# Performance work log

Measured on AMD Instinct MI355X. Metric: run time of the kernel, lower is better.

## Reference

```python
import jax, jax.numpy as jnp
import numpy as np

B, T, H = 8, 512, 1024
DC = 8            # concept_dim_total = 6 + 2
DIN = H + DC      # 1032
V, L = 8, 4       # op_vocab_size, prog_len


def setup_inputs() -> dict:
    key = jax.random.key(0)
    ks = jax.random.split(key, 20)
    s = 0.02
    inp = {
        "x": jax.random.normal(ks[0], (B, T, H), dtype=jnp.float32),
        # concept classifier heads
        "W_tt": jax.random.normal(ks[1], (6, H), dtype=jnp.float32) * s,
        "b_tt": jnp.zeros((6,), jnp.float32),
        "W_pol": jax.random.normal(ks[2], (2, H), dtype=jnp.float32) * s,
        "b_pol": jnp.zeros((2,), jnp.float32),
        # program generator
        "W_c2h": jax.random.normal(ks[3], (H, DIN), dtype=jnp.float32) * s,
        "b_c2h": jnp.zeros((H,), jnp.float32),
        "W_ih": jax.random.normal(ks[4], (3 * H, DIN), dtype=jnp.float32) * s,
        "W_hh": jax.random.normal(ks[5], (3 * H, H), dtype=jnp.float32) * s,
        "b_ih": jnp.zeros((3 * H,), jnp.float32),
        "b_hh": jnp.zeros((3 * H,), jnp.float32),
        "W_proj": jax.random.normal(ks[6], (V, H), dtype=jnp.float32) * s,
        "b_proj": jnp.zeros((V,), jnp.float32),
        # op library: num_ops stacked Linear(DIN->H)-GELU-Linear(H->H)
        "W1": jax.random.normal(ks[7], (V, H, DIN), dtype=jnp.float32) * s,
        "b1": jnp.zeros((V, H), jnp.float32),
        "W2": jax.random.normal(ks[8], (V, H, H), dtype=jnp.float32) * s,
        "b2": jnp.zeros((V, H), jnp.float32),
    }
    return inp


def _forward(x, W_tt, b_tt, W_pol, b_pol, W_c2h, b_c2h, W_ih, W_hh, b_ih, b_hh,
             W_proj, b_proj, W1, b1, W2, b2):
    # concept classifier
    tt = x @ W_tt.T + b_tt              # (B,T,6)
    pol = x @ W_pol.T + b_pol           # (B,T,2)
    concept_feats = jnp.concatenate([tt, pol], axis=-1)  # (B,T,8)
    concept_summary = jnp.concatenate([tt.mean(axis=1), pol.mean(axis=1)], axis=-1)  # (B,8)
    pooled = x.mean(axis=1)             # (B,H)
    context = jnp.concatenate([pooled, concept_summary], axis=-1)  # (B,DIN)

    # program generator: GRU with zero inputs, h0 from context (PyTorch gate eqs)
    h0 = context @ W_c2h.T + b_c2h      # (B,H)
    zero_in = jnp.zeros((context.shape[0], DIN), x.dtype)
    gi = zero_in @ W_ih.T + b_ih        # (B,3H); zero-input contribution = bias
    gi_r, gi_z, gi_n = jnp.split(gi, 3, axis=-1)

    def gru_step(h, _):
        gh = h @ W_hh.T + b_hh
        gh_r, gh_z, gh_n = jnp.split(gh, 3, axis=-1)
        r = jax.nn.sigmoid(gi_r + gh_r)
        z = jax.nn.sigmoid(gi_z + gh_z)
        n = jnp.tanh(gi_n + r * gh_n)
        h_new = (1.0 - z) * n + z * h
        return h_new, h_new

    _, hs = jax.lax.scan(gru_step, h0, None, length=L)   # (L,B,H)
    rnn_out = jnp.transpose(hs, (1, 0, 2))               # (B,L,H)
    program_logits = rnn_out @ W_proj.T + b_proj         # (B,L,V)

    # op library: outputs are identical across L, so compute each op once and
    # average the softmax weights over L (exact same math as expand+mean).
    x_aug = jnp.concatenate([x, concept_feats], axis=-1)           # (B,T,DIN)
    hmid = jax.nn.gelu(jnp.einsum('btd,vhd->btvh', x_aug, W1) + b1, approximate=False)
    op_out = jnp.einsum('btvh,voh->btvo', hmid, W2) + b2           # (B,T,V,H)
    w = jax.nn.softmax(program_logits, axis=-1).mean(axis=1)       # (B,V)
    out = jnp.einsum('btvd,bv->btd', op_out, w)                    # (B,T,H)
    return out, program_logits, tt, pol, pooled


def reference(x, W_tt, b_tt, W_pol, b_pol, W_c2h, b_c2h, W_ih, W_hh, b_ih, b_hh,
              W_proj, b_proj, W1, b1, W2, b2):
    return _forward(x, W_tt, b_tt, W_pol, b_pol, W_c2h, b_c2h, W_ih, W_hh,
                    b_ih, b_hh, W_proj, b_proj, W1, b1, W2, b2)
```

## Files before the change

### kernel.cpp

```cpp
#include <hip/hip_runtime.h>
#include <hip/hip_bf16.h>
#include <math.h>

typedef __bf16 bf16;
typedef __bf16 bf16x8 __attribute__((ext_vector_type(8)));
typedef float f32x4 __attribute__((ext_vector_type(4)));


__device__ __forceinline__ float wsum(float v) {
#pragma unroll
  for (int off = 32; off; off >>= 1) v += __shfl_xor(v, off, 64);
  return v;
}

__device__ __forceinline__ void g2l16(const bf16* g, bf16* l) {
  __builtin_amdgcn_global_load_lds(
      (__attribute__((address_space(1))) void*)g,
      (__attribute__((address_space(3))) void*)l, 16, 0, 0);
}

__device__ __forceinline__ bf16x8 pack8(float4 a, float4 b) {
  bf16x8 r;
  r[0] = (bf16)a.x; r[1] = (bf16)a.y; r[2] = (bf16)a.z; r[3] = (bf16)a.w;
  r[4] = (bf16)b.x; r[5] = (bf16)b.y; r[6] = (bf16)b.z; r[7] = (bf16)b.w;
  return r;
}

__device__ __forceinline__ float gelu_fast(float x) {
  float s = __builtin_fabsf(x) * 0.70710678118654752f;
  float t = __builtin_amdgcn_rcpf(__builtin_fmaf(0.3275911f, s, 1.0f));
  float p = __builtin_fmaf(t, 1.061405429f, -1.453152027f);
  p = __builtin_fmaf(t, p, 1.421413741f);
  p = __builtin_fmaf(t, p, -0.284496736f);
  p = __builtin_fmaf(t, p, 0.254829592f);
  float e = exp2f(s * s * -1.4426950408889634f);
  float erf_abs = __builtin_fmaf(-p * t, e, 1.0f);
  return __builtin_fmaf(0.5f * __builtin_fabsf(x), erf_abs, 0.5f * x);
}

template <int DCT>
__global__ void k_front_t(const float* __restrict__ x,
                          const float* __restrict__ Wtt, const float* __restrict__ btt,
                          const float* __restrict__ Wpol, const float* __restrict__ bpol,
                          float* __restrict__ out_tt, float* __restrict__ out_pol,
                          float* __restrict__ feats, bf16* __restrict__ xbE,
                          int H, int KE, long BT, int C1, int C2) {
  int wave = threadIdx.x >> 6, lane = threadIdx.x & 63;
  long m = (long)blockIdx.x * 4 + wave;
  if (m >= BT) return;
  const float* xp = x + m * H;
  bf16* dp = xbE + m * KE;
  const float* wp[DCT];
#pragma unroll
  for (int c = 0; c < DCT; c++)
    wp[c] = (c < C1) ? (Wtt + (size_t)c * H) : (Wpol + (size_t)(c - C1) * H);
  float acc[DCT];
#pragma unroll
  for (int c = 0; c < DCT; c++) acc[c] = 0.f;
  for (int e = lane * 8; e + 8 <= H; e += 512) {
    float4 a = *(const float4*)(xp + e);
    float4 b = *(const float4*)(xp + e + 4);
    *(bf16x8*)(dp + e) = pack8(a, b);
#pragma unroll
    for (int c = 0; c < DCT; c++) {
      float4 wa = *(const float4*)(wp[c] + e);
      float4 wb = *(const float4*)(wp[c] + e + 4);
      acc[c] += a.x * wa.x + a.y * wa.y + a.z * wa.z + a.w * wa.w +
                b.x * wb.x + b.y * wb.y + b.z * wb.z + b.w * wb.w;
    }
  }
#pragma unroll
  for (int c = 0; c < DCT; c++) acc[c] = wsum(acc[c]);
  float fv = 0.f;
#pragma unroll
  for (int c = 0; c < DCT; c++) fv = (lane == c) ? acc[c] : fv;
  if (lane < DCT) {
    fv += (lane < C1) ? btt[lane] : bpol[lane - C1];
    if (lane < C1) out_tt[m * C1 + lane] = fv;
    else           out_pol[m * C2 + (lane - C1)] = fv;
    feats[m * DCT + lane] = fv;
  }
  int pad = KE - H;
  if (lane < pad) dp[H + lane] = (lane < DCT) ? (bf16)fv : (bf16)0.f;
}

__global__ void k_feats_g(const float* __restrict__ x,
                          const float* __restrict__ Wtt, const float* __restrict__ btt,
                          const float* __restrict__ Wpol, const float* __restrict__ bpol,
                          float* __restrict__ out_tt, float* __restrict__ out_pol,
                          float* __restrict__ feats,
                          int H, int T, int BT, int C1, int C2) {
  int wave = threadIdx.x >> 6, lane = threadIdx.x & 63;
  int site = blockIdx.x * 4 + wave;
  if (site >= BT) return;
  int DC = C1 + C2;
  const float* xp = x + (size_t)site * H;
  for (int c = 0; c < DC; c++) {
    const float* wr = (c < C1) ? (Wtt + (size_t)c * H) : (Wpol + (size_t)(c - C1) * H);
    float a = 0.f;
    for (int k = lane; k < H; k += 64) a += xp[k] * wr[k];
    a = wsum(a);
    if (lane == 0) {
      float val = a + (c < C1 ? btt[c] : bpol[c - C1]);
      if (c < C1) out_tt[(size_t)site * C1 + c] = val;
      else        out_pol[(size_t)site * C2 + (c - C1)] = val;
      feats[(size_t)site * DC + c] = val;
    }
  }
}

__global__ void k_xext(const float* __restrict__ x, const float* __restrict__ feats,
                       bf16* __restrict__ xbE, int H, int KE, int DC, long BT) {
  int wave = threadIdx.x >> 6, lane = threadIdx.x & 63;
  long m = (long)blockIdx.x * 4 + wave;
  if (m >= BT) return;
  const float* xp = x + m * H;
  bf16* dp = xbE + m * KE;
  for (int e = lane * 8; e + 8 <= H; e += 512) {
    float4 a = *(const float4*)(xp + e);
    float4 b = *(const float4*)(xp + e + 4);
    *(bf16x8*)(dp + e) = pack8(a, b);
  }
  int pad = KE - H;
  if (lane < pad)
    dp[H + lane] = (lane < DC) ? (bf16)feats[m * DC + lane] : (bf16)0.f;
}

__global__ void k_prep(const float* __restrict__ W1, bf16* __restrict__ W1bE,
                       const float* __restrict__ W2, bf16* __restrict__ W2b,
                       int H, int DIN, int KE, int DC, long N2, int nW1, long nCvtThreads) {
  int wave = threadIdx.x >> 6, lane = threadIdx.x & 63;
  if (blockIdx.x < (unsigned)nW1) {
    long n = (long)blockIdx.x * 4 + wave;
    if (n >= N2) return;
    const float* sp = W1 + n * DIN;
    bf16* dp = W1bE + n * KE;
    for (int e = lane * 8; e + 8 <= H; e += 512) {
      float4 a = *(const float4*)(sp + e);
      float4 b = *(const float4*)(sp + e + 4);
      *(bf16x8*)(dp + e) = pack8(a, b);
    }
    int pad = KE - H;
    if (lane < pad)
      dp[H + lane] = (lane < DC) ? (bf16)sp[H + lane] : (bf16)0.f;
  } else {
    long n = N2 * (long)H;
    for (long i = (long)(blockIdx.x - nW1) * 256 + threadIdx.x; i * 8 < n;
         i += nCvtThreads) {
      long e = i * 8;
      if (e + 8 <= n) {
        float4 a = *(const float4*)(W2 + e);
        float4 b = *(const float4*)(W2 + e + 4);
        *(bf16x8*)(W2b + e) = pack8(a, b);
      } else {
        for (long j = e; j < n; j++) W2b[j] = (bf16)W2[j];
      }
    }
  }
}

__global__ void k_stats(const float* __restrict__ x, float* __restrict__ pooled,
                        const float* __restrict__ feats, float* __restrict__ fsum,
                        int H, int T, int tsplit, int DC, int BDC, int poolBlocks) {
  int wave = threadIdx.x >> 6, lane = threadIdx.x & 63;
  if (blockIdx.x < (unsigned)poolBlocks) {
    int hBlocks = (H + 255) / 256;
    int bs = blockIdx.x / tsplit, ts = blockIdx.x % tsplit;
    int b = bs / hBlocks;
    int h = (bs % hBlocks) * 256 + threadIdx.x;
    if (h >= H) return;
    int tlo = (int)(((long)T * ts) / tsplit), thi = (int)(((long)T * (ts + 1)) / tsplit);
    const float* p = x + (size_t)b * T * H + h;
    float s = 0.f;
    for (int t = tlo; t < thi; t++) s += p[(size_t)t * H];
    atomicAdd(&pooled[(size_t)b * H + h], s / (float)T);
  } else {
    int r = (blockIdx.x - poolBlocks) * 4 + wave;
    if (r >= BDC) return;
    int b = r / DC, c = r % DC;
    const float* p = feats + ((size_t)b * T) * DC + c;
    float a = 0.f;
    for (int t = lane; t < T; t += 64) a += p[(size_t)t * DC];
    a = wsum(a);
    if (lane == 0) fsum[r] = a / (float)T;
  }
}

__global__ void k_ctx_h0(const float* __restrict__ Wc2h, const float* __restrict__ bc2h,
                         const float* __restrict__ pooled, const float* __restrict__ fmean,
                         float* __restrict__ h0, float* __restrict__ out_pool,
                         int H, int DIN, int B, int DC) {
  int wave = threadIdx.x >> 6, lane = threadIdx.x & 63;
  int r = blockIdx.x * 4 + wave;
  if (r >= B * H) return;
  int b = r / H, j = r % H;
  const float* wrow = Wc2h + (size_t)j * DIN;
  float a = 0.f;
  for (int k = lane; k < DIN; k += 64) {
    float cv = (k < H) ? pooled[(size_t)b * H + k] : fmean[b * DC + (k - H)];
    a += cv * wrow[k];
  }
  a = wsum(a);
  if (lane == 0) {
    h0[r] = a + bc2h[j];
    out_pool[r] = pooled[r];
  }
}

__global__ void k_gru(const float* __restrict__ hin, const float* __restrict__ Whh,
                      const float* __restrict__ bih, const float* __restrict__ bhh,
                      float* __restrict__ hout, float* __restrict__ hsl,
                      int H, int B) {
  int wave = threadIdx.x >> 6, lane = threadIdx.x & 63;
  int r = blockIdx.x * 4 + wave;
  if (r >= B * H) return;
  int b = r / H, j = r % H;
  const float* h = hin + (size_t)b * H;
  const float* w0 = Whh + (size_t)j * H;
  const float* w1 = Whh + (size_t)(H + j) * H;
  const float* w2 = Whh + (size_t)(2 * H + j) * H;
  float ar = 0, az = 0, an = 0;
  for (int k = lane; k < H; k += 64) {
    float hv = h[k];
    ar += hv * w0[k];
    az += hv * w1[k];
    an += hv * w2[k];
  }
  ar = wsum(ar); az = wsum(az); an = wsum(an);
  if (lane == 0) {
    float ghr = ar + bhh[j];
    float ghz = az + bhh[H + j];
    float ghn = an + bhh[2 * H + j];
    float rg = 1.f / (1.f + expf(-(bih[j] + ghr)));
    float zg = 1.f / (1.f + expf(-(bih[H + j] + ghz)));
    float ng = tanhf(bih[2 * H + j] + rg * ghn);
    float hn = (1.f - zg) * ng + zg * h[j];
    hout[r] = hn;
    hsl[r] = hn;
  }
}

__global__ void k_logits(const float* __restrict__ hs, const float* __restrict__ Wproj,
                         const float* __restrict__ bproj, float* __restrict__ logits,
                         float* __restrict__ out_log, int H, int B, int L, int V) {
  int wave = threadIdx.x >> 6, lane = threadIdx.x & 63;
  int r = blockIdx.x * 4 + wave;
  if (r >= B * L * V) return;
  int b = r / (L * V), rem = r % (L * V), l = rem / V, u = rem % V;
  const float* h = hs + ((size_t)l * B + b) * H;
  const float* w = Wproj + (size_t)u * H;
  float a = 0.f;
  for (int k = lane; k < H; k += 64) a += h[k] * w[k];
  a = wsum(a);
  if (lane == 0) {
    a += bproj[u];
    int idx = (b * L + l) * V + u;
    logits[idx] = a;
    out_log[idx] = a;
  }
}

__global__ void k_wmix(const float* __restrict__ logits, const float* __restrict__ b2,
                       float* __restrict__ wv, float* __restrict__ wb2,
                       int B, int L, int V, int H) {
  __shared__ float sm[2048];
  __shared__ float wsh[512];
  int t = threadIdx.x;
  if (t < B * L) {
    const float* lg = logits + t * V;
    float mx = lg[0];
    for (int u = 1; u < V; u++) mx = fmaxf(mx, lg[u]);
    float s = 0.f;
    for (int u = 0; u < V; u++) s += expf(lg[u] - mx);
    for (int u = 0; u < V; u++) sm[t * V + u] = expf(lg[u] - mx) / s;
  }
  __syncthreads();
  if (t < B * V) {
    int b = t / V, u = t % V;
    float a = 0.f;
    for (int l = 0; l < L; l++) a += sm[(b * L + l) * V + u];
    a /= (float)L;
    wsh[t] = a;
    wv[t] = a;
  }
  __syncthreads();
  for (int idx = t; idx < B * H; idx += 256) {
    int b = idx / H, o = idx % H;
    float a = 0.f;
    for (int u = 0; u < V; u++) a += wsh[b * V + u] * b2[(size_t)u * H + o];
    wb2[idx] = a;
  }
}

__global__ __launch_bounds__(256, 2) void gemm1_mfma(
    const bf16* __restrict__ A, const bf16* __restrict__ Bb, bf16* __restrict__ hmid,
    const float* __restrict__ b1, const float* __restrict__ wv,
    int rows, long moff, int KE, int H, int N, int T, int V) {
  __shared__ __align__(16) bf16 As[128 * 64];
  __shared__ __align__(16) bf16 Bs[128 * 64];
  const int wave = threadIdx.x >> 6, lane = threadIdx.x & 63;
  int bx = blockIdx.x, by = blockIdx.y;
  if (gridDim.x == 64 && (gridDim.y & 3) == 0) {
    int f = by * 64 + bx;
    int xcd = f & 7, q = f >> 3;
    int cs = q >> 5, t = q & 31;
    bx = xcd * 8 + (t & 7);
    by = cs * 4 + (t >> 3);
  }
  const int m0 = by * 128, n0 = bx * 128;
  const int mw = (wave >> 1) * 64, nw = (wave & 1) * 64;
  const int rr = lane >> 3;
  const int srcOff = ((lane & 7) ^ rr) << 3;
  const int rA = lane & 15, q4 = lane >> 4;
  f32x4 acc[4][4];
#pragma unroll
  for (int i = 0; i < 4; i++)
#pragma unroll
    for (int j = 0; j < 4; j++) acc[i][j] = (f32x4){0.f, 0.f, 0.f, 0.f};

  int arow[4], brow[4];
#pragma unroll
  for (int t = 0; t < 4; ++t) {
    int r = wave * 32 + t * 8 + rr;
    arow[t] = (m0 + r < rows) ? (m0 + r) : (rows - 1);
    brow[t] = (n0 + r < N) ? (n0 + r) : (N - 1);
  }

  for (int k0 = 0; k0 < KE; k0 += 64) {
    __syncthreads();
#pragma unroll
    for (int t = 0; t < 4; ++t) {
      int c = wave * 4 + t;
      g2l16(A + (size_t)arow[t] * KE + k0 + srcOff, &As[c * 512]);
      g2l16(Bb + (size_t)brow[t] * KE + k0 + srcOff, &Bs[c * 512]);
    }
    __syncthreads();
#pragma unroll
    for (int kk = 0; kk < 2; ++kk) {
      bf16x8 af[4], bfr[4];
#pragma unroll
      for (int i = 0; i < 4; i++) {
        int row = mw + i * 16 + rA;
        af[i] = *(const bf16x8*)&As[row * 64 + ((((kk << 2) + q4) ^ (row & 7)) << 3)];
      }
#pragma unroll
      for (int j = 0; j < 4; j++) {
        int row = nw + j * 16 + rA;
        bfr[j] = *(const bf16x8*)&Bs[row * 64 + ((((kk << 2) + q4) ^ (row & 7)) << 3)];
      }
#pragma unroll
      for (int i = 0; i < 4; i++)
#pragma unroll
        for (int j = 0; j < 4; j++)
          acc[i][j] = __builtin_amdgcn_mfma_f32_16x16x32_bf16(af[i], bfr[j], acc[i][j], 0, 0, 0);
    }
  }

  int vj[4];
  float b1j[4];
#pragma unroll
  for (int j = 0; j < 4; j++) {
    int n = n0 + nw + j * 16 + rA;
    if (n >= N) n = N - 1;
    vj[j] = n / H;
    b1j[j] = b1[n];
  }
  int bBase = ((T & 127) == 0) ? (int)((moff + m0) / T) : -1;
  float wfac[4];
#pragma unroll
  for (int j = 0; j < 4; j++)
    wfac[j] = (bBase >= 0) ? wv[bBase * V + vj[j]] : 0.f;
#pragma unroll
  for (int i = 0; i < 4; i++) {
#pragma unroll
    for (int r = 0; r < 4; r++) {
      int m = m0 + mw + i * 16 + q4 * 4 + r;
      if (m >= rows) continue;
      long gm = moff + m;
      int bb = (bBase >= 0) ? bBase : (int)(gm / T);
#pragma unroll
      for (int j = 0; j < 4; j++) {
        int n = n0 + nw + j * 16 + rA;
        if (n >= N) continue;
        float val = gelu_fast(acc[i][j][r] + b1j[j]);
        float wf = (bBase >= 0) ? wfac[j] : wv[bb * V + vj[j]];
        hmid[(size_t)m * N + n] = (bf16)(val * wf);
      }
    }
  }
}

__global__ __launch_bounds__(256, 2) void gemm2_mfma(
    const bf16* __restrict__ A, const bf16* __restrict__ W2b, float* __restrict__ part,
    long partStride, int rows, int H, int K, int kchunk) {
  __shared__ __align__(16) bf16 As[128 * 64];
  __shared__ __align__(16) bf16 Bs[128 * 64];
  const int wave = threadIdx.x >> 6, lane = threadIdx.x & 63;
  int bx = blockIdx.x, by = blockIdx.y;
  if (gridDim.x == 8 && (gridDim.y & 31) == 0) {
    int f = by * 8 + bx;
    int xcd = f & 7, q = f >> 3;
    int cs = q >> 5, t = q & 31;
    bx = t & 7;
    by = (xcd + (cs << 3)) * 4 + (t >> 3);
  }
  const int m0 = by * 128, n0 = bx * 128;
  const int mw = (wave >> 1) * 64, nw = (wave & 1) * 64;
  const int rr = lane >> 3;
  const int srcOff = ((lane & 7) ^ rr) << 3;
  const int rA = lane & 15, q4 = lane >> 4;
  int kz0 = blockIdx.z * kchunk;
  int kz1 = kz0 + kchunk; if (kz1 > K) kz1 = K;
  if (kz0 >= K) return;
  f32x4 acc[4][4];
#pragma unroll
  for (int i = 0; i < 4; i++)
#pragma unroll
    for (int j = 0; j < 4; j++) acc[i][j] = (f32x4){0.f, 0.f, 0.f, 0.f};

  int arow[4], brow[4];
#pragma unroll
  for (int t = 0; t < 4; ++t) {
    int r = wave * 32 + t * 8 + rr;
    arow[t] = (m0 + r < rows) ? (m0 + r) : (rows - 1);
    brow[t] = (n0 + r < H) ? (n0 + r) : (H - 1);
  }

  int kv = kz0 / H, kh = kz0 % H;
  for (int k0 = kz0; k0 < kz1; k0 += 64) {
    const bf16* Bk = W2b + (size_t)kv * H * H + kh;
    __syncthreads();
#pragma unroll
    for (int t = 0; t < 4; ++t) {
      int c = wave * 4 + t;
      g2l16(A + (size_t)arow[t] * K + k0 + srcOff, &As[c * 512]);
      g2l16(Bk + (size_t)brow[t] * H + srcOff, &Bs[c * 512]);
    }
    __syncthreads();
#pragma unroll
    for (int kk = 0; kk < 2; ++kk) {
      bf16x8 af[4], bfr[4];
#pragma unroll
      for (int i = 0; i < 4; i++) {
        int row = mw + i * 16 + rA;
        af[i] = *(const bf16x8*)&As[row * 64 + ((((kk << 2) + q4) ^ (row & 7)) << 3)];
      }
#pragma unroll
      for (int j = 0; j < 4; j++) {
        int row = nw + j * 16 + rA;
        bfr[j] = *(const bf16x8*)&Bs[row * 64 + ((((kk << 2) + q4) ^ (row & 7)) << 3)];
      }
#pragma unroll
      for (int i = 0; i < 4; i++)
#pragma unroll
        for (int j = 0; j < 4; j++)
          acc[i][j] = __builtin_amdgcn_mfma_f32_16x16x32_bf16(af[i], bfr[j], acc[i][j], 0, 0, 0);
    }
    kh += 64;
    if (kh >= H) { kh = 0; kv++; }
  }

  float* pz = part + (size_t)blockIdx.z * partStride;
#pragma unroll
  for (int i = 0; i < 4; i++) {
#pragma unroll
    for (int r = 0; r < 4; r++) {
      int m = m0 + mw + i * 16 + q4 * 4 + r;
      if (m >= rows) continue;
#pragma unroll
      for (int j = 0; j < 4; j++) {
        int n = n0 + nw + j * 16 + rA;
        if (n >= H) continue;
        pz[(size_t)m * H + n] = acc[i][j][r];
      }
    }
  }
}

__global__ void k_red(const float* __restrict__ part, const float* __restrict__ wb2,
                      float* __restrict__ outY, long moff, int rows, long partStride,
                      int H, int T, int ZS) {
  int wave = threadIdx.x >> 6, lane = threadIdx.x & 63;
  long m = (long)blockIdx.x * 4 + wave;
  if (m >= rows) return;
  long gm = moff + m;
  int b = (int)(gm / T);
  const float* w = wb2 + (size_t)b * H;
  float* d = outY + (size_t)gm * H;
  for (int e = lane * 4; e + 4 <= H; e += 256) {
    float4 s = *(const float4*)(w + e);
    for (int z = 0; z < ZS; z++) {
      float4 p = *(const float4*)(part + (size_t)z * partStride + (size_t)m * H + e);
      s.x += p.x; s.y += p.y; s.z += p.z; s.w += p.w;
    }
    *(float4*)(d + e) = s;
  }
}

extern "C" void kernel_launch(void* const* d_in, const int* in_sizes, int n_in,
                              void* d_out, int out_size, void* d_ws, size_t ws_size,
                              hipStream_t stream) {
  const float* x      = (const float*)d_in[0];
  const float* W_tt   = (const float*)d_in[1];
  const float* b_tt   = (const float*)d_in[2];
  const float* W_pol  = (const float*)d_in[3];
  const float* b_pol  = (const float*)d_in[4];
  const float* W_c2h  = (const float*)d_in[5];
  const float* b_c2h  = (const float*)d_in[6];
  const float* W_hh   = (const float*)d_in[8];
  const float* b_ih   = (const float*)d_in[9];
  const float* b_hh   = (const float*)d_in[10];
  const float* W_proj = (const float*)d_in[11];
  const float* b_proj = (const float*)d_in[12];
  const float* W1     = (const float*)d_in[13];
  const float* b1     = (const float*)d_in[14];
  const float* W2     = (const float*)d_in[15];
  const float* b2     = (const float*)d_in[16];
  float* out = (float*)d_out;
  char* ws = (char*)d_ws;

  const int C1 = in_sizes[2];
  const int C2 = in_sizes[4];
  const int H  = in_sizes[1] / C1;
  const int DC = C1 + C2;
  const int DIN = H + DC;
  const int V  = in_sizes[12];
  const long BT = (long)in_sizes[0] / H;
  long R = (long)out_size - BT * (long)(H + DC);
  int B = 0, L = 0;
  for (int Lc = 1; Lc <= 32; ++Lc) {
    long den = (long)Lc * V + H;
    if (R % den == 0) {
      long Bc = R / den;
      if (Bc >= 1 && BT % Bc == 0) {
        if (B == 0 || Lc == 4) { B = (int)Bc; L = Lc; }
        if (Lc == 4) break;
      }
    }
  }
  if (B == 0) { B = 8; L = 4; }
  const int T = (int)(BT / B);
  const long N2 = (long)V * H;
  const int KE = H + 64;
  const int ZS = 4;

  size_t o = 0;
  auto alloc = [&](size_t bytes) { size_t r = o; o = (o + bytes + 255) & ~(size_t)255; return r; };
  float* feats  = (float*)(ws + alloc((size_t)BT * DC * 4));
  size_t off_pooled = alloc((size_t)B * H * 4);
  float* pooled = (float*)(ws + off_pooled);
  float* fsum   = (float*)(ws + alloc((size_t)B * DC * 4));
  float* hbuf   = (float*)(ws + alloc((size_t)2 * B * H * 4));
  float* hs     = (float*)(ws + alloc((size_t)L * B * H * 4));
  float* logits = (float*)(ws + alloc((size_t)B * L * V * 4));
  float* wv     = (float*)(ws + alloc((size_t)B * V * 4));
  float* wb2    = (float*)(ws + alloc((size_t)B * H * 4));
  bf16* xbE  = (bf16*)(ws + alloc((size_t)BT * KE * 2));
  bf16* W1bE = (bf16*)(ws + alloc((size_t)N2 * KE * 2));
  bf16* W2b  = (bf16*)(ws + alloc((size_t)N2 * H * 2));
  size_t off_hmid = alloc(0);
  long rowBytes = N2 * 2 + (long)ZS * H * 4;
  long avail = (long)ws_size - (long)off_hmid;
  long Mc = ((avail / rowBytes) / 128) * 128;
  long bt128 = ((BT + 127) / 128) * 128;
  if (Mc > bt128) Mc = bt128;
  if (Mc < 128) Mc = 128;
  bf16* hmid = (bf16*)(ws + off_hmid);
  float* part = (float*)(ws + off_hmid + (size_t)Mc * N2 * 2);
  long partStride = Mc * (long)H;

  float* out_y    = out;
  float* out_log  = out_y + (size_t)BT * H;
  float* out_tt   = out_log + (size_t)B * L * V;
  float* out_pol  = out_tt + (size_t)BT * C1;
  float* out_pool = out_pol + (size_t)BT * C2;

  hipMemsetAsync(ws + off_pooled, 0, (size_t)B * H * 4, stream);

  int nW1 = (int)((N2 + 3) / 4);
  int nCvt = 1024;
  k_prep<<<nW1 + nCvt, 256, 0, stream>>>(W1, W1bE, W2, W2b, H, DIN, KE, DC, N2,
                                         nW1, (long)nCvt * 256);
  if (DC == 8 && (H & 1023) == 0) {
    k_front_t<8><<<(int)((BT + 3) / 4), 256, 0, stream>>>(x, W_tt, b_tt, W_pol, b_pol,
                                                          out_tt, out_pol, feats, xbE,
                                                          H, KE, BT, C1, C2);
  } else {
    k_feats_g<<<(int)((BT + 3) / 4), 256, 0, stream>>>(x, W_tt, b_tt, W_pol, b_pol,
                                                       out_tt, out_pol, feats,
                                                       H, T, (int)BT, C1, C2);
    k_xext<<<(int)((BT + 3) / 4), 256, 0, stream>>>(x, feats, xbE, H, KE, DC, BT);
  }
  int hBlocks = (H + 255) / 256;
  int poolBlocks = B * hBlocks * 8;
  int fsumBlocks = (B * DC + 3) / 4;
  k_stats<<<poolBlocks + fsumBlocks, 256, 0, stream>>>(x, pooled, feats, fsum,
                                                       H, T, 8, DC, B * DC, poolBlocks);
  k_ctx_h0<<<(B * H + 3) / 4, 256, 0, stream>>>(W_c2h, b_c2h, pooled, fsum,
                                                hbuf, out_pool, H, DIN, B, DC);
  float* hA = hbuf;
  float* hB = hbuf + (size_t)B * H;
  for (int l = 0; l < L; ++l) {
    k_gru<<<(B * H + 3) / 4, 256, 0, stream>>>((l & 1) ? hB : hA, W_hh, b_ih, b_hh,
                                               (l & 1) ? hA : hB, hs + (size_t)l * B * H,
                                               H, B);
  }
  k_logits<<<(B * L * V + 3) / 4, 256, 0, stream>>>(hs, W_proj, b_proj, logits,
                                                    out_log, H, B, L, V);
  k_wmix<<<1, 256, 0, stream>>>(logits, b2, wv, wb2, B, L, V, H);

  int kchunk = (int)((((N2 / ZS) + 63) / 64) * 64);
  for (long moff = 0; moff < BT; moff += Mc) {
    int rows = (int)(((BT - moff) < Mc) ? (BT - moff) : Mc);
    dim3 g1((unsigned)((N2 + 127) / 128), (unsigned)((rows + 127) / 128));
    dim3 g2((unsigned)((H + 127) / 128), (unsigned)((rows + 127) / 128), ZS);
    gemm1_mfma<<<g1, 256, 0, stream>>>(xbE + (size_t)moff * KE, W1bE, hmid, b1, wv,
                                       rows, moff, KE, H, (int)N2, T, V);
    gemm2_mfma<<<g2, 256, 0, stream>>>(hmid, W2b, part, partStride,
                                       rows, H, (int)N2, kchunk);
    k_red<<<(int)((rows + 3) / 4), 256, 0, stream>>>(part, wb2, out_y, moff, rows,
                                                     partStride, H, T, ZS);
  }
}
```

Baseline: 454.9 us.

## Double-buffer LDS tiles in both MFMA GEMMs with async prefetch pipeline

Both GEMM kernels now keep two LDS buffers for A and B. The next K tile is fetched with global_load_lds while the current tile is computed, and explicit vmcnt waits plus raw barriers replace the two __syncthreads per iteration, so global-load latency can overlap MFMA work. LDS use doubles to 64KB per block, which may limit the two-blocks-per-CU occupancy target. The front kernel is also reworked: the bf16 conversion loop is split from the concept dot products, which now run over float4 chunks with a stride of 256.

```diff
diff --git a/kernel.cpp b/kernel.cpp
--- a/kernel.cpp
+++ b/kernel.cpp
@@ -50,23 +50,24 @@
   if (m >= BT) return;
   const float* xp = x + m * H;
   bf16* dp = xbE + m * KE;
-  const float* wp[DCT];
-#pragma unroll
-  for (int c = 0; c < DCT; c++)
-    wp[c] = (c < C1) ? (Wtt + (size_t)c * H) : (Wpol + (size_t)(c - C1) * H);
-  float acc[DCT];
-#pragma unroll
-  for (int c = 0; c < DCT; c++) acc[c] = 0.f;
   for (int e = lane * 8; e + 8 <= H; e += 512) {
     float4 a = *(const float4*)(xp + e);
     float4 b = *(const float4*)(xp + e + 4);
     *(bf16x8*)(dp + e) = pack8(a, b);
+  }
+  const float* wp[DCT];
+#pragma unroll
+  for (int c = 0; c < DCT; c++)
+    wp[c] = (c < C1) ? (Wtt + (size_t)c * H) : (Wpol + (size_t)(c - C1) * H);
+  float acc[DCT];
+#pragma unroll
+  for (int c = 0; c < DCT; c++) acc[c] = 0.f;
+  for (int k = lane * 4; k < H; k += 256) {
+    float4 xv = *(const float4*)(xp + k);
 #pragma unroll
     for (int c = 0; c < DCT; c++) {
-      float4 wa = *(const float4*)(wp[c] + e);
-      float4 wb = *(const float4*)(wp[c] + e + 4);
-      acc[c] += a.x * wa.x + a.y * wa.y + a.z * wa.z + a.w * wa.w +
-                b.x * wb.x + b.y * wb.y + b.z * wb.z + b.w * wb.w;
+      float4 wv4 = *(const float4*)(wp[c] + k);
+      acc[c] += xv.x * wv4.x + xv.y * wv4.y + xv.z * wv4.z + xv.w * wv4.w;
     }
   }
 #pragma unroll
@@ -296,8 +297,8 @@
     const bf16* __restrict__ A, const bf16* __restrict__ Bb, bf16* __restrict__ hmid,
     const float* __restrict__ b1, const float* __restrict__ wv,
     int rows, long moff, int KE, int H, int N, int T, int V) {
-  __shared__ __align__(16) bf16 As[128 * 64];
-  __shared__ __align__(16) bf16 Bs[128 * 64];
+  __shared__ __align__(16) bf16 As[2][128 * 64];
+  __shared__ __align__(16) bf16 Bs[2][128 * 64];
   const int wave = threadIdx.x >> 6, lane = threadIdx.x & 63;
   int bx = blockIdx.x, by = blockIdx.y;
   if (gridDim.x == 64 && (gridDim.y & 3) == 0) {
@@ -326,27 +327,30 @@
     brow[t] = (n0 + r < N) ? (n0 + r) : (N - 1);
   }
 
-  for (int k0 = 0; k0 < KE; k0 += 64) {
-    __syncthreads();
+  const int NT = KE >> 6;
+  int k0s = 0;
+  auto STAGE = [&](int bsel) {
 #pragma unroll
     for (int t = 0; t < 4; ++t) {
       int c = wave * 4 + t;
-      g2l16(A + (size_t)arow[t] * KE + k0 + srcOff, &As[c * 512]);
-      g2l16(Bb + (size_t)brow[t] * KE + k0 + srcOff, &Bs[c * 512]);
-    }
-    __syncthreads();
+      g2l16(A + (size_t)arow[t] * KE + k0s + srcOff, &As[bsel][c * 512]);
+      g2l16(Bb + (size_t)brow[t] * KE + k0s + srcOff, &Bs[bsel][c * 512]);
+    }
+    k0s += 64;
+  };
+  auto COMPUTE = [&](int bsel) {
 #pragma unroll
     for (int kk = 0; kk < 2; ++kk) {
       bf16x8 af[4], bfr[4];
 #pragma unroll
       for (int i = 0; i < 4; i++) {
         int row = mw + i * 16 + rA;
-        af[i] = *(const bf16x8*)&As[row * 64 + ((((kk << 2) + q4) ^ (row & 7)) << 3)];
+        af[i] = *(const bf16x8*)&As[bsel][row * 64 + ((((kk << 2) + q4) ^ (row & 7)) << 3)];
       }
 #pragma unroll
       for (int j = 0; j < 4; j++) {
         int row = nw + j * 16 + rA;
-        bfr[j] = *(const bf16x8*)&Bs[row * 64 + ((((kk << 2) + q4) ^ (row & 7)) << 3)];
+        bfr[j] = *(const bf16x8*)&Bs[bsel][row * 64 + ((((kk << 2) + q4) ^ (row & 7)) << 3)];
       }
 #pragma unroll
       for (int i = 0; i < 4; i++)
@@ -354,7 +358,35 @@
         for (int j = 0; j < 4; j++)
           acc[i][j] = __builtin_amdgcn_mfma_f32_16x16x32_bf16(af[i], bfr[j], acc[i][j], 0, 0, 0);
     }
-  }
+  };
+
+  STAGE(0);
+  if (NT > 1) {
+    STAGE(1);
+    asm volatile("s_waitcnt vmcnt(8)" ::: "memory");
+  } else {
+    asm volatile("s_waitcnt vmcnt(0)" ::: "memory");
+  }
+  __builtin_amdgcn_s_barrier();
+  int cur = 0, t = 0;
+  for (; t + 2 < NT; ++t) {
+    COMPUTE(cur);
+    asm volatile("" ::: "memory");
+    __builtin_amdgcn_s_barrier();
+    STAGE(cur);
+    asm volatile("s_waitcnt vmcnt(8)" ::: "memory");
+    __builtin_amdgcn_s_barrier();
+    cur ^= 1;
+  }
+  if (t + 1 < NT) {
+    COMPUTE(cur);
+    asm volatile("" ::: "memory");
+    __builtin_amdgcn_s_barrier();
+    asm volatile("s_waitcnt vmcnt(0)" ::: "memory");
+    __builtin_amdgcn_s_barrier();
+    cur ^= 1;
+  }
+  COMPUTE(cur);
 
   int vj[4];
   float b1j[4];
@@ -393,8 +425,8 @@
 __global__ __launch_bounds__(256, 2) void gemm2_mfma(
     const bf16* __restrict__ A, const bf16* __restrict__ W2b, float* __restrict__ part,
     long partStride, int rows, int H, int K, int kchunk) {
-  __shared__ __align__(16) bf16 As[128 * 64];
-  __shared__ __align__(16) bf16 Bs[128 * 64];
+  __shared__ __align__(16) bf16 As[2][128 * 64];
+  __shared__ __align__(16) bf16 Bs[2][128 * 64];
   const int wave = threadIdx.x >> 6, lane = threadIdx.x & 63;
   int bx = blockIdx.x, by = blockIdx.y;
   if (gridDim.x == 8 && (gridDim.y & 31) == 0) {
@@ -426,29 +458,31 @@
     brow[t] = (n0 + r < H) ? (n0 + r) : (H - 1);
   }
 
-  int kv = kz0 / H, kh = kz0 % H;
-  for (int k0 = kz0; k0 < kz1; k0 += 64) {
-    const bf16* Bk = W2b + (size_t)kv * H * H + kh;
-    __syncthreads();
+  const int NT = (kz1 - kz0) >> 6;
+  int k0s = kz0, kvs = kz0 / H, khs = kz0 % H;
+  auto STAGE = [&](int bsel) {
+    const bf16* Bk = W2b + (size_t)kvs * H * H + khs;
 #pragma unroll
     for (int t = 0; t < 4; ++t) {
       int c = wave * 4 + t;
-      g2l16(A + (size_t)arow[t] * K + k0 + srcOff, &As[c * 512]);
-      g2l16(Bk + (size_t)brow[t] * H + srcOff, &Bs[c * 512]);
-    }
-    __syncthreads();
+      g2l16(A + (size_t)arow[t] * K + k0s + srcOff, &As[bsel][c * 512]);
+      g2l16(Bk + (size_t)brow[t] * H + srcOff, &Bs[bsel][c * 512]);
+    }
+    k0s += 64; khs += 64; if (khs >= H) { khs = 0; kvs++; }
+  };
+  auto COMPUTE = [&](int bsel) {
 #pragma unroll
     for (int kk = 0; kk < 2; ++kk) {
       bf16x8 af[4], bfr[4];
 #pragma unroll
       for (int i = 0; i < 4; i++) {
         int row = mw + i * 16 + rA;
-        af[i] = *(const bf16x8*)&As[row * 64 + ((((kk << 2) + q4) ^ (row & 7)) << 3)];
+        af[i] = *(const bf16x8*)&As[bsel][row * 64 + ((((kk << 2) + q4) ^ (row & 7)) << 3)];
       }
 #pragma unroll
       for (int j = 0; j < 4; j++) {
         int row = nw + j * 16 + rA;
-        bfr[j] = *(const bf16x8*)&Bs[row * 64 + ((((kk << 2) + q4) ^ (row & 7)) << 3)];
+        bfr[j] = *(const bf16x8*)&Bs[bsel][row * 64 + ((((kk << 2) + q4) ^ (row & 7)) << 3)];
       }
 #pragma unroll
       for (int i = 0; i < 4; i++)
@@ -456,9 +490,35 @@
         for (int j = 0; j < 4; j++)
           acc[i][j] = __builtin_amdgcn_mfma_f32_16x16x32_bf16(af[i], bfr[j], acc[i][j], 0, 0, 0);
     }
-    kh += 64;
-    if (kh >= H) { kh = 0; kv++; }
-  }
+  };
+
+  STAGE(0);
+  if (NT > 1) {
+    STAGE(1);
+    asm volatile("s_waitcnt vmcnt(8)" ::: "memory");
+  } else {
+    asm volatile("s_waitcnt vmcnt(0)" ::: "memory");
+  }
+  __builtin_amdgcn_s_barrier();
+  int cur = 0, t = 0;
+  for (; t + 2 < NT; ++t) {
+    COMPUTE(cur);
+    asm volatile("" ::: "memory");
+    __builtin_amdgcn_s_barrier();
+    STAGE(cur);
+    asm volatile("s_waitcnt vmcnt(8)" ::: "memory");
+    __builtin_amdgcn_s_barrier();
+    cur ^= 1;
+  }
+  if (t + 1 < NT) {
+    COMPUTE(cur);
+    asm volatile("" ::: "memory");
+    __builtin_amdgcn_s_barrier();
+    asm volatile("s_waitcnt vmcnt(0)" ::: "memory");
+    __builtin_amdgcn_s_barrier();
+    cur ^= 1;
+  }
+  COMPUTE(cur);
 
   float* pz = part + (size_t)blockIdx.z * partStride;
 #pragma unroll
```

Result: slower. 475.3 us (+4.5%).

## Fuse stats, h0, GRU steps, logits and softmax mix into one cooperative kernel

Applied to the files above, without the earlier changes.

Replaces the chain of small launches (pooling stats, context-to-h0, four GRU step kernels, logits, weight mix) with a single cooperative kernel of 256 blocks that uses grid-wide syncs between phases. The goal is to remove per-launch overhead and the memset on the latency-bound RNN path. In exchange each GRU row is computed by fewer waves, and grid.sync adds its own cost. The front kernel is also reordered so the bf16 copy pass and the concept dot-product pass run as separate loops with float4 strides.

```diff
diff --git a/kernel.cpp b/kernel.cpp
--- a/kernel.cpp
+++ b/kernel.cpp
@@ -1,6 +1,9 @@
 #include <hip/hip_runtime.h>
+#include <hip/hip_cooperative_groups.h>
 #include <hip/hip_bf16.h>
 #include <math.h>
+
+namespace cg = cooperative_groups;
 
 typedef __bf16 bf16;
 typedef __bf16 bf16x8 __attribute__((ext_vector_type(8)));
@@ -50,23 +53,24 @@
   if (m >= BT) return;
   const float* xp = x + m * H;
   bf16* dp = xbE + m * KE;
-  const float* wp[DCT];
-#pragma unroll
-  for (int c = 0; c < DCT; c++)
-    wp[c] = (c < C1) ? (Wtt + (size_t)c * H) : (Wpol + (size_t)(c - C1) * H);
-  float acc[DCT];
-#pragma unroll
-  for (int c = 0; c < DCT; c++) acc[c] = 0.f;
   for (int e = lane * 8; e + 8 <= H; e += 512) {
     float4 a = *(const float4*)(xp + e);
     float4 b = *(const float4*)(xp + e + 4);
     *(bf16x8*)(dp + e) = pack8(a, b);
+  }
+  const float* wp[DCT];
+#pragma unroll
+  for (int c = 0; c < DCT; c++)
+    wp[c] = (c < C1) ? (Wtt + (size_t)c * H) : (Wpol + (size_t)(c - C1) * H);
+  float acc[DCT];
+#pragma unroll
+  for (int c = 0; c < DCT; c++) acc[c] = 0.f;
+  for (int k = lane * 4; k < H; k += 256) {
+    float4 xv = *(const float4*)(xp + k);
 #pragma unroll
     for (int c = 0; c < DCT; c++) {
-      float4 wa = *(const float4*)(wp[c] + e);
-      float4 wb = *(const float4*)(wp[c] + e + 4);
-      acc[c] += a.x * wa.x + a.y * wa.y + a.z * wa.z + a.w * wa.w +
-                b.x * wb.x + b.y * wb.y + b.z * wb.z + b.w * wb.w;
+      float4 wv4 = *(const float4*)(wp[c] + k);
+      acc[c] += xv.x * wv4.x + xv.y * wv4.y + xv.z * wv4.z + xv.w * wv4.w;
     }
   }
 #pragma unroll
@@ -155,6 +159,141 @@
       } else {
         for (long j = e; j < n; j++) W2b[j] = (bf16)W2[j];
       }
+    }
+  }
+}
+
+__global__ void k_rnn(const float* __restrict__ x, const float* __restrict__ feats,
+                      float* __restrict__ pooledPart, float* __restrict__ pooled,
+                      float* __restrict__ fsum,
+                      const float* __restrict__ Wc2h, const float* __restrict__ bc2h,
+                      const float* __restrict__ Whh, const float* __restrict__ bih,
+                      const float* __restrict__ bhh,
+                      const float* __restrict__ Wproj, const float* __restrict__ bproj,
+                      const float* __restrict__ b2,
+                      float* __restrict__ hbuf, float* __restrict__ hs,
+                      float* __restrict__ out_log, float* __restrict__ wv,
+                      float* __restrict__ wb2, float* __restrict__ out_pool,
+                      int H, int DIN, int T, int B, int DC, int L, int V) {
+  cg::grid_group grid = cg::this_grid();
+  __shared__ float sm[256];
+  __shared__ float wsh[64];
+  const int bl = blockIdx.x, tid = threadIdx.x;
+  const int wave = tid >> 6, lane = tid & 63;
+  const int gw = bl * 4 + wave;
+
+  {
+    int b = bl >> 5, ts = (bl >> 2) & 7, hc = bl & 3;
+    int h = hc * 256 + tid;
+    int tlo = (int)(((long)T * ts) / 8), thi = (int)(((long)T * (ts + 1)) / 8);
+    const float* p = x + ((size_t)b * T + tlo) * H + h;
+    float s = 0.f;
+    for (int t = tlo; t < thi; t++, p += H) s += *p;
+    pooledPart[((size_t)ts * B + b) * H + h] = s;
+  }
+  grid.sync();
+  {
+    int idx = bl * 256 + tid;
+    if (idx < B * H) {
+      float s = 0.f;
+      for (int ts = 0; ts < 8; ts++) s += pooledPart[(size_t)ts * B * H + idx];
+      s /= (float)T;
+      pooled[idx] = s;
+      out_pool[idx] = s;
+    }
+    int r = (bl - 32) * 4 + wave;
+    if (bl >= 32 && r < B * DC) {
+      int b = r / DC, c = r % DC;
+      const float* p = feats + ((size_t)b * T) * DC + c;
+      float a = 0.f;
+      for (int t = lane; t < T; t += 64) a += p[(size_t)t * DC];
+      a = wsum(a);
+      if (lane == 0) fsum[r] = a / (float)T;
+    }
+  }
+  grid.sync();
+  float* hA = hbuf;
+  float* hB = hbuf + (size_t)B * H;
+  for (int w = 0; w < 8; w++) {
+    int r = gw * 8 + w;
+    if (r >= B * H) break;
+    int b = r / H, j = r % H;
+    const float* wrow = Wc2h + (size_t)j * DIN;
+    float a = 0.f;
+    for (int k = lane; k < DIN; k += 64) {
+      float cv = (k < H) ? pooled[(size_t)b * H + k] : fsum[b * DC + (k - H)];
+      a += cv * wrow[k];
+    }
+    a = wsum(a);
+    if (lane == 0) hA[r] = a + bc2h[j];
+  }
+  grid.sync();
+  for (int l = 0; l < L; l++) {
+    const float* hin = (l & 1) ? hB : hA;
+    float* hout = (l & 1) ? hA : hB;
+    for (int w = 0; w < 8; w++) {
+      int r = gw * 8 + w;
+      if (r >= B * H) break;
+      int b = r / H, j = r % H;
+      const float* h = hin + (size_t)b * H;
+      const float* w0 = Whh + (size_t)j * H;
+      const float* w1 = Whh + (size_t)(H + j) * H;
+      const float* w2 = Whh + (size_t)(2 * H + j) * H;
+      float ar = 0, az = 0, an = 0;
+      for (int k = lane; k < H; k += 64) {
+        float hv = h[k];
+        ar += hv * w0[k];
+        az += hv * w1[k];
+        an += hv * w2[k];
+      }
+      ar = wsum(ar); az = wsum(az); an = wsum(an);
+      if (lane == 0) {
+        float ghr = ar + bhh[j];
+        float ghz = az + bhh[H + j];
+        float ghn = an + bhh[2 * H + j];
+        float rg = 1.f / (1.f + expf(-(bih[j] + ghr)));
+        float zg = 1.f / (1.f + expf(-(bih[H + j] + ghz)));
+        float ng = tanhf(bih[2 * H + j] + rg * ghn);
+        float hn = (1.f - zg) * ng + zg * h[j];
+        hout[r] = hn;
+        hs[(size_t)l * B * H + r] = hn;
+      }
+    }
+    grid.sync();
+  }
+  if (gw < B * L * V) {
+    int b = gw / (L * V), rem = gw % (L * V), l = rem / V, u = rem % V;
+    const float* h = hs + ((size_t)l * B + b) * H;
+    const float* wp = Wproj + (size_t)u * H;
+    float a = 0.f;
+    for (int k = lane; k < H; k += 64) a += h[k] * wp[k];
+    a = wsum(a);
+    if (lane == 0) out_log[(b * L + l) * V + u] = a + bproj[u];
+  }
+  grid.sync();
+  if (bl < B) {
+    int b = bl;
+    if (tid < L) {
+      const float* lg = out_log + (b * L + tid) * V;
+      float mx = lg[0];
+      for (int u = 1; u < V; u++) mx = fmaxf(mx, lg[u]);
+      float s = 0.f;
+      for (int u = 0; u < V; u++) s += expf(lg[u] - mx);
+      for (int u = 0; u < V; u++) sm[tid * V + u] = expf(lg[u] - mx) / s;
+    }
+    __syncthreads();
+    if (tid < V) {
+      float a = 0.f;
+      for (int l = 0; l < L; l++) a += sm[l * V + tid];
+      a /= (float)L;
+      wsh[tid] = a;
+      wv[b * V + tid] = a;
+    }
+    __syncthreads();
+    for (int o = tid; o < H; o += 256) {
+      float a = 0.f;
+      for (int u = 0; u < V; u++) a += wsh[u] * b2[(size_t)u * H + o];
+      wb2[(size_t)b * H + o] = a;
     }
   }
 }
@@ -550,6 +689,7 @@
   size_t off_pooled = alloc((size_t)B * H * 4);
   float* pooled = (float*)(ws + off_pooled);
   float* fsum   = (float*)(ws + alloc((size_t)B * DC * 4));
+  float* pooledPart = (float*)(ws + alloc((size_t)8 * B * H * 4));
   float* hbuf   = (float*)(ws + alloc((size_t)2 * B * H * 4));
   float* hs     = (float*)(ws + alloc((size_t)L * B * H * 4));
   float* logits = (float*)(ws + alloc((size_t)B * L * V * 4));
@@ -575,13 +715,12 @@
   float* out_pol  = out_tt + (size_t)BT * C1;
   float* out_pool = out_pol + (size_t)BT * C2;
 
-  hipMemsetAsync(ws + off_pooled, 0, (size_t)B * H * 4, stream);
-
   int nW1 = (int)((N2 + 3) / 4);
   int nCvt = 1024;
   k_prep<<<nW1 + nCvt, 256, 0, stream>>>(W1, W1bE, W2, W2b, H, DIN, KE, DC, N2,
                                          nW1, (long)nCvt * 256);
-  if (DC == 8 && (H & 1023) == 0) {
+  bool frontFused = (DC == 8 && (H & 1023) == 0);
+  if (frontFused) {
     k_front_t<8><<<(int)((BT + 3) / 4), 256, 0, stream>>>(x, W_tt, b_tt, W_pol, b_pol,
                                                           out_tt, out_pol, feats, xbE,
                                                           H, KE, BT, C1, C2);
@@ -591,23 +730,37 @@
                                                        H, T, (int)BT, C1, C2);
     k_xext<<<(int)((BT + 3) / 4), 256, 0, stream>>>(x, feats, xbE, H, KE, DC, BT);
   }
-  int hBlocks = (H + 255) / 256;
-  int poolBlocks = B * hBlocks * 8;
-  int fsumBlocks = (B * DC + 3) / 4;
-  k_stats<<<poolBlocks + fsumBlocks, 256, 0, stream>>>(x, pooled, feats, fsum,
-                                                       H, T, 8, DC, B * DC, poolBlocks);
-  k_ctx_h0<<<(B * H + 3) / 4, 256, 0, stream>>>(W_c2h, b_c2h, pooled, fsum,
-                                                hbuf, out_pool, H, DIN, B, DC);
-  float* hA = hbuf;
-  float* hB = hbuf + (size_t)B * H;
-  for (int l = 0; l < L; ++l) {
-    k_gru<<<(B * H + 3) / 4, 256, 0, stream>>>((l & 1) ? hB : hA, W_hh, b_ih, b_hh,
-                                               (l & 1) ? hA : hB, hs + (size_t)l * B * H,
-                                               H, B);
-  }
-  k_logits<<<(B * L * V + 3) / 4, 256, 0, stream>>>(hs, W_proj, b_proj, logits,
-                                                    out_log, H, B, L, V);
-  k_wmix<<<1, 256, 0, stream>>>(logits, b2, wv, wb2, B, L, V, H);
+
+  bool coop = (B == 8 && H == 1024 && DC == 8 && V == 8 && L == 4 && T >= 8);
+  if (coop) {
+    void* args[] = {
+      (void*)&x, (void*)&feats, (void*)&pooledPart, (void*)&pooled, (void*)&fsum,
+      (void*)&W_c2h, (void*)&b_c2h, (void*)&W_hh, (void*)&b_ih, (void*)&b_hh,
+      (void*)&W_proj, (void*)&b_proj, (void*)&b2,
+      (void*)&hbuf, (void*)&hs, (void*)&out_log, (void*)&wv, (void*)&wb2,
+      (void*)&out_pool,
+      (void*)&H, (void*)&DIN, (void*)&T, (void*)&B, (void*)&DC, (void*)&L, (void*)&V};
+    hipLaunchCooperativeKernel((const void*)k_rnn, dim3(256), dim3(256), args, 0, stream);
+  } else {
+    hipMemsetAsync(ws + off_pooled, 0, (size_t)B * H * 4, stream);
+    int hBlocks = (H + 255) / 256;
+    int poolBlocks = B * hBlocks * 8;
+    int fsumBlocks = (B * DC + 3) / 4;
+    k_stats<<<poolBlocks + fsumBlocks, 256, 0, stream>>>(x, pooled, feats, fsum,
+                                                         H, T, 8, DC, B * DC, poolBlocks);
+    k_ctx_h0<<<(B * H + 3) / 4, 256, 0, stream>>>(W_c2h, b_c2h, pooled, fsum,
+                                                  hbuf, out_pool, H, DIN, B, DC);
+    float* hA = hbuf;
+    float* hB = hbuf + (size_t)B * H;
+    for (int l = 0; l < L; ++l) {
+      k_gru<<<(B * H + 3) / 4, 256, 0, stream>>>((l & 1) ? hB : hA, W_hh, b_ih, b_hh,
+                                                 (l & 1) ? hA : hB, hs + (size_t)l * B * H,
+                                                 H, B);
+    }
+    k_logits<<<(B * L * V + 3) / 4, 256, 0, stream>>>(hs, W_proj, b_proj, logits,
+                                                      out_log, H, B, L, V);
+    k_wmix<<<1, 256, 0, stream>>>(logits, b2, wv, wb2, B, L, V, H);
+  }
 
   int kchunk = (int)((((N2 / ZS) + 63) / 64) * 64);
   for (long moff = 0; moff < BT; moff += Mc) {
```

Result: slower. 824.5 us (+81.2%).
